# Kernel optimization log

Measured on AMD Instinct MI355X. Metric: run time of the kernel, lower is better.

## Reference

```python
import jax, jax.numpy as jnp
import numpy as np

OUT = (7, 7, 7)      # output_size (D_out, H_out, W_out)
SCALE = 1.0          # spatial_scale


def setup_inputs() -> dict:
    key = jax.random.key(0)
    k1, k2 = jax.random.split(key)
    B, C, D, H, W = 2, 256, 64, 64, 64
    N = 512
    features = jax.random.normal(k1, (B, C, D, H, W), dtype=jnp.float32)
    p = jax.random.uniform(k2, (B, N, 6), dtype=jnp.float32) * 63.0
    lo = jnp.minimum(p[..., :3], p[..., 3:])
    hi = jnp.maximum(p[..., :3], p[..., 3:])
    proposals = jnp.concatenate([lo, hi], axis=-1)  # (B, N, 6) valid boxes
    return {"features": features, "proposals": proposals}


def _trilinear(vol, gz, gy, gx):
    # vol: (C, D, H, W); gz/gy/gx: (Do, Ho, Wo) voxel-space coords.
    # grid_sample(mode='bilinear', padding_mode='zeros', align_corners=True)
    C, D, H, W = vol.shape
    z0f, y0f, x0f = jnp.floor(gz), jnp.floor(gy), jnp.floor(gx)
    wz, wy, wx = gz - z0f, gy - y0f, gx - x0f
    z0, y0, x0 = z0f.astype(jnp.int32), y0f.astype(jnp.int32), x0f.astype(jnp.int32)

    def gather(zi, yi, xi):
        valid = (zi >= 0) & (zi < D) & (yi >= 0) & (yi < H) & (xi >= 0) & (xi < W)
        v = vol[:, jnp.clip(zi, 0, D - 1), jnp.clip(yi, 0, H - 1), jnp.clip(xi, 0, W - 1)]
        return v * valid.astype(vol.dtype)[None]  # (C, Do, Ho, Wo)

    out = jnp.zeros((C,) + gz.shape, dtype=vol.dtype)
    for dz in (0, 1):
        for dy in (0, 1):
            for dx in (0, 1):
                w = ((wz if dz else 1.0 - wz)
                     * (wy if dy else 1.0 - wy)
                     * (wx if dx else 1.0 - wx))
                out = out + gather(z0 + dz, y0 + dy, x0 + dx) * w[None]
    return out


def reference(features, proposals):
    # features: (B, C, D, H, W); proposals: (B, N, 6) [x1,y1,z1,x2,y2,z2]
    B, C, D, H, W = features.shape
    Do, Ho, Wo = OUT

    def one_roi(vol, prop):
        p = prop * SCALE
        x1, y1, z1, x2, y2, z2 = p[0], p[1], p[2], p[3], p[4], p[5]
        zc = jnp.linspace(z1, z2, Do)
        yc = jnp.linspace(y1, y2, Ho)
        xc = jnp.linspace(x1, x2, Wo)
        gz, gy, gx = jnp.meshgrid(zc, yc, xc, indexing='ij')  # (Do,Ho,Wo)
        return _trilinear(vol, gz, gy, gx)  # (C, Do, Ho, Wo)

    per_batch = jax.vmap(lambda vol, props: jax.vmap(lambda p: one_roi(vol, p))(props))
    out = per_batch(features, proposals)  # (B, N, C, Do, Ho, Wo)
    return out.reshape(B * proposals.shape[1], C, Do, Ho, Wo)
```

## Files before the change

kernel.cpp:

```cpp
#include <hip/hip_runtime.h>
#include <hip/hip_fp16.h>


#define B_      2
#define C_      256
#define N_      512
#define NENT    (N_ * 7)
#define SP      66
#define THREADS 512
#define GROUPS  10
#define REC_F_BASE 128
#define WS_NEEDED ((size_t)REC_F_BASE * 4 + (size_t)B_ * NENT * 8 * 4)

typedef _Float16 h2v __attribute__((ext_vector_type(2)));

__device__ __forceinline__ float gcoord(float lo, float hi, int i) {
    return lo + (hi - lo) * (1.0f / 6.0f) * (float)i;
}

__device__ __forceinline__ uint32_t pkrtz(float a, float b) {
    auto h = __builtin_amdgcn_cvt_pkrtz(a, b);
    return __builtin_bit_cast(uint32_t, h);
}

__device__ __forceinline__ float xlerp(uint32_t pkv, uint32_t pkw) {
#if __has_builtin(__builtin_amdgcn_fdot2)
    return __builtin_amdgcn_fdot2(__builtin_bit_cast(h2v, pkv),
                                  __builtin_bit_cast(h2v, pkw), 0.0f, false);
#else
    h2v v = __builtin_bit_cast(h2v, pkv);
    h2v w = __builtin_bit_cast(h2v, pkw);
    return (float)v[0] * (float)w[0] + (float)v[1] * (float)w[1];
#endif
}

__global__ __launch_bounds__(256) void bucket_kernel(
    const float* __restrict__ props, int* __restrict__ wsi, float* __restrict__ wsf)
{
    int b = blockIdx.x;
    __shared__ int counts[63];
    __shared__ int starts[64];
    __shared__ int cursors[63];
    int tid = threadIdx.x;
    if (tid < 63) counts[tid] = 0;
    __syncthreads();
    for (int e = tid; e < NENT; e += 256) {
        int n = e / 7, iz = e - n * 7;
        const float* pr = props + (size_t)(b * N_ + n) * 6;
        float gz = gcoord(pr[2], pr[5], iz);
        int z0 = min(max((int)gz, 0), 62);
        atomicAdd(&counts[z0], 1);
    }
    __syncthreads();
    if (tid == 0) {
        int s = 0;
        for (int k = 0; k < 63; ++k) { starts[k] = s; s += counts[k]; }
        starts[63] = s;
    }
    __syncthreads();
    if (tid < 63) cursors[tid] = starts[tid];
    __syncthreads();
    for (int e = tid; e < NENT; e += 256) {
        int n = e / 7, iz = e - n * 7;
        const float* pr = props + (size_t)(b * N_ + n) * 6;
        float x1p = pr[0], y1p = pr[1], z1p = pr[2];
        float x2p = pr[3], y2p = pr[4], z2p = pr[5];
        float gz = gcoord(z1p, z2p, iz);
        int z0 = min(max((int)gz, 0), 62);
        float wz = gz - (float)z0;
        int pos = atomicAdd(&cursors[z0], 1);
        int off = (b * N_ + n) * (C_ * 343) + iz * 49;
        float* r = wsf + REC_F_BASE + (size_t)(b * NENT + pos) * 8;
        r[0] = x1p; r[1] = (x2p - x1p) * (1.0f / 6.0f);
        r[2] = y1p; r[3] = (y2p - y1p) * (1.0f / 6.0f);
        r[4] = wz;  r[5] = __int_as_float(off);
        r[6] = 0.0f; r[7] = 0.0f;
    }
    if (tid < 64) wsi[b * 64 + tid] = starts[tid];
}

__global__ __launch_bounds__(THREADS, 8) void roialign3d_small_kernel(
    const float* __restrict__ feat,
    const int* __restrict__ wsi,
    const float* __restrict__ wsf,
    float* __restrict__ out)
{
    __shared__ __align__(16) uint2 pk2[64 * SP];

    int bid = blockIdx.x;
    int s   = bid & 511;
    int z0  = bid >> 9;
    int b   = s >> 8;
    int c   = s & 255;
    int tid = threadIdx.x;

    int base = wsi[b * 64 + z0];
    int end  = wsi[b * 64 + z0 + 1];
    if (base == end) return;

    const float* vol = feat + ((size_t)s << 18) + ((size_t)z0 << 12);

    int y  = tid >> 3;
    int x8 = (tid & 7) << 3;
    const float* src = vol + y * 64 + x8;
    float4 p0a = *(const float4*)(src);
    float4 p0b = *(const float4*)(src + 4);
    float4 p1a = *(const float4*)(src + 4096);
    float4 p1b = *(const float4*)(src + 4100);

    int g = tid / 49;
    int p = tid - g * 49;
    int iy = p / 7;
    float fx = (float)(p - iy * 7);
    float fy = (float)iy;
    const float4* recs = (const float4*)(wsf + REC_F_BASE);
    const int rbase = b * NENT;
    int myEnd = (g < GROUPS) ? end : base;
    int e = base + g;
    float4 rA, rB, rAn, rBn;
    if (e < myEnd) {
        rA = recs[(size_t)(rbase + e) * 2];
        rB = recs[(size_t)(rbase + e) * 2 + 1];
        if (e + GROUPS < myEnd) {
            rAn = recs[(size_t)(rbase + e + GROUPS) * 2];
            rBn = recs[(size_t)(rbase + e + GROUPS) * 2 + 1];
        }
    }

    {
        float n0 = __shfl_down(p0a.x, 1);
        float n1 = __shfl_down(p1a.x, 1);
        uint4* d = (uint4*)&pk2[y * SP + x8];
        uint4 w0, w1, w2, w3;
        w0.x = pkrtz(p0a.x, p0a.y); w0.y = pkrtz(p1a.x, p1a.y);
        w0.z = pkrtz(p0a.y, p0a.z); w0.w = pkrtz(p1a.y, p1a.z);
        w1.x = pkrtz(p0a.z, p0a.w); w1.y = pkrtz(p1a.z, p1a.w);
        w1.z = pkrtz(p0a.w, p0b.x); w1.w = pkrtz(p1a.w, p1b.x);
        w2.x = pkrtz(p0b.x, p0b.y); w2.y = pkrtz(p1b.x, p1b.y);
        w2.z = pkrtz(p0b.y, p0b.z); w2.w = pkrtz(p1b.y, p1b.z);
        w3.x = pkrtz(p0b.z, p0b.w); w3.y = pkrtz(p1b.z, p1b.w);
        w3.z = pkrtz(p0b.w, n0);    w3.w = pkrtz(p1b.w, n1);
        d[0] = w0; d[1] = w1; d[2] = w2; d[3] = w3;
    }
    __syncthreads();

    float* outc = out + (size_t)c * 343;
    while (e < myEnd) {
        float gx = fmaf(rA.y, fx, rA.x);
        float gy = fmaf(rA.w, fy, rA.z);
        int x0 = (int)gx, y0 = (int)gy;
        float wx = __builtin_amdgcn_fractf(gx);
        float wy = __builtin_amdgcn_fractf(gy);
        uint32_t pw = pkrtz(1.0f - wx, wx);
        float wz = rB.x;
        int offc = __float_as_int(rB.y);
        int sl = y0 * SP + x0;
        uint2 q0 = pk2[sl];
        uint2 q1 = pk2[sl + SP];

        float4 tA = rAn, tB = rBn;
        int e2 = e + 2 * GROUPS;
        if (e2 < myEnd) {
            rAn = recs[(size_t)(rbase + e2) * 2];
            rBn = recs[(size_t)(rbase + e2) * 2 + 1];
        }

        float c00 = xlerp(q0.x, pw);
        float c10 = xlerp(q0.y, pw);
        float c01 = xlerp(q1.x, pw);
        float c11 = xlerp(q1.y, pw);
        float d0 = fmaf(c01 - c00, wy, c00);
        float d1 = fmaf(c11 - c10, wy, c10);
        outc[offc + p] = fmaf(d1 - d0, wz, d0);

        e += GROUPS; rA = tA; rB = tB;
    }
}

__global__ __launch_bounds__(128) void roialign3d_fallback(
    const float* __restrict__ feat, const float* __restrict__ props,
    float* __restrict__ out)
{
    int bid = blockIdx.x;
    int xcd = bid & 7;
    int j   = bid >> 3;
    int s   = xcd + ((j >> 9) << 3);
    int n   = j & 511;
    int b   = s >> 8;
    int c   = s & 255;
    const float* prop = props + ((size_t)(b * N_ + n)) * 6;
    float x1p = prop[0], y1p = prop[1], z1p = prop[2];
    float x2p = prop[3], y2p = prop[4], z2p = prop[5];
    float sx = (x2p - x1p) * (1.0f / 6.0f);
    float sy = (y2p - y1p) * (1.0f / 6.0f);
    float sz = (z2p - z1p) * (1.0f / 6.0f);
    const float* vol = feat + (size_t)s * (64 * 64 * 64);
    float* o = out + ((size_t)(b * N_ + n) * C_ + c) * 343;
    for (int p = threadIdx.x; p < 343; p += 128) {
        int iz = p / 49, r = p - iz * 49, iy = r / 7, ix = r - iy * 7;
        float gx = x1p + sx * ix, gy = y1p + sy * iy, gz = z1p + sz * iz;
        int x0 = (int)gx, y0 = (int)gy, z0 = (int)gz;
        float wx = gx - x0, wy = gy - y0, wz = gz - z0;
        int x1 = min(x0 + 1, 63), y1 = min(y0 + 1, 63), z1 = min(z0 + 1, 63);
        const float* p00 = vol + ((z0 * 64 + y0) << 6);
        const float* p01 = vol + ((z0 * 64 + y1) << 6);
        const float* p10 = vol + ((z1 * 64 + y0) << 6);
        const float* p11 = vol + ((z1 * 64 + y1) << 6);
        float c00 = p00[x0] + (p00[x1] - p00[x0]) * wx;
        float c01 = p01[x0] + (p01[x1] - p01[x0]) * wx;
        float c10 = p10[x0] + (p10[x1] - p10[x0]) * wx;
        float c11 = p11[x0] + (p11[x1] - p11[x0]) * wx;
        float d0 = c00 + (c01 - c00) * wy;
        float d1 = c10 + (c11 - c10) * wy;
        o[p] = d0 + (d1 - d0) * wz;
    }
}

extern "C" void kernel_launch(void* const* d_in, const int* in_sizes, int n_in,
                              void* d_out, int out_size, void* d_ws, size_t ws_size,
                              hipStream_t stream) {
    const float* feat  = (const float*)d_in[0];
    const float* props = (const float*)d_in[1];
    float* out = (float*)d_out;

    if (ws_size < WS_NEEDED) {
        roialign3d_fallback<<<B_ * C_ * N_, 128, 0, stream>>>(feat, props, out);
        return;
    }
    int*   wsi = (int*)d_ws;
    float* wsf = (float*)d_ws;
    bucket_kernel<<<B_, 256, 0, stream>>>(props, wsi, wsf);
    roialign3d_small_kernel<<<63 * 512, THREADS, 0, stream>>>(feat, wsi, wsf, out);
}
```

Measured before the change: 301.4 us.

## Map each thread to a full output row of seven x-samples per entry

The sampling kernel now gives each thread a whole 7-wide x-row of one (roi, z-slice) entry, instead of a single output voxel per thread with 10 groups of 49. Each wave covers 9 entries × 7 rows, so a 512-thread block handles 72 entries per iteration rather than 10. Since buckets average roughly 57 entries, most blocks should finish in one pass, with fewer record loads and less loop overhead, and the unrolled 7-point loop adds more independent work per thread. In exchange, each store instruction within a wave now writes addresses strided by 7 floats instead of contiguous ones, and register pressure rises.

```diff
diff --git a/kernel.cpp b/kernel.cpp
--- a/kernel.cpp
+++ b/kernel.cpp
@@ -8,7 +8,7 @@
 #define NENT    (N_ * 7)
 #define SP      66
 #define THREADS 512
-#define GROUPS  10
+#define EPP     72
 #define REC_F_BASE 128
 #define WS_NEEDED ((size_t)REC_F_BASE * 4 + (size_t)B_ * NENT * 8 * 4)
 
@@ -79,7 +79,7 @@
     if (tid < 64) wsi[b * 64 + tid] = starts[tid];
 }
 
-__global__ __launch_bounds__(THREADS, 8) void roialign3d_small_kernel(
+__global__ __launch_bounds__(THREADS, 8) void roialign3d_row_kernel(
     const float* __restrict__ feat,
     const int* __restrict__ wsi,
     const float* __restrict__ wsf,
@@ -108,22 +108,22 @@
     float4 p1a = *(const float4*)(src + 4096);
     float4 p1b = *(const float4*)(src + 4100);
 
-    int g = tid / 49;
-    int p = tid - g * 49;
-    int iy = p / 7;
-    float fx = (float)(p - iy * 7);
+    int wid  = tid >> 6;
+    int lane = tid & 63;
+    int g    = lane / 7;
+    int iy   = lane - g * 7;
     float fy = (float)iy;
     const float4* recs = (const float4*)(wsf + REC_F_BASE);
     const int rbase = b * NENT;
-    int myEnd = (g < GROUPS) ? end : base;
-    int e = base + g;
+    int myEnd = (lane < 63) ? end : base;
+    int e = base + wid * 9 + g;
     float4 rA, rB, rAn, rBn;
     if (e < myEnd) {
         rA = recs[(size_t)(rbase + e) * 2];
         rB = recs[(size_t)(rbase + e) * 2 + 1];
-        if (e + GROUPS < myEnd) {
-            rAn = recs[(size_t)(rbase + e + GROUPS) * 2];
-            rBn = recs[(size_t)(rbase + e + GROUPS) * 2 + 1];
+        if (e + EPP < myEnd) {
+            rAn = recs[(size_t)(rbase + e + EPP) * 2];
+            rBn = recs[(size_t)(rbase + e + EPP) * 2 + 1];
         }
     }
 
@@ -146,34 +146,41 @@
 
     float* outc = out + (size_t)c * 343;
     while (e < myEnd) {
-        float gx = fmaf(rA.y, fx, rA.x);
-        float gy = fmaf(rA.w, fy, rA.z);
-        int x0 = (int)gx, y0 = (int)gy;
-        float wx = __builtin_amdgcn_fractf(gx);
-        float wy = __builtin_amdgcn_fractf(gy);
-        uint32_t pw = pkrtz(1.0f - wx, wx);
-        float wz = rB.x;
-        int offc = __float_as_int(rB.y);
-        int sl = y0 * SP + x0;
-        uint2 q0 = pk2[sl];
-        uint2 q1 = pk2[sl + SP];
+        float gx0 = rA.x, sx = rA.y;
+        float gy  = fmaf(rA.w, fy, rA.z);
+        int   y0  = (int)gy;
+        float wy  = __builtin_amdgcn_fractf(gy);
+        float wz  = rB.x;
+        int  offc = __float_as_int(rB.y);
+        int slrow = y0 * SP;
+        float* od = outc + offc + iy * 7;
 
         float4 tA = rAn, tB = rBn;
-        int e2 = e + 2 * GROUPS;
+        int e2 = e + 2 * EPP;
         if (e2 < myEnd) {
             rAn = recs[(size_t)(rbase + e2) * 2];
             rBn = recs[(size_t)(rbase + e2) * 2 + 1];
         }
 
-        float c00 = xlerp(q0.x, pw);
-        float c10 = xlerp(q0.y, pw);
-        float c01 = xlerp(q1.x, pw);
-        float c11 = xlerp(q1.y, pw);
-        float d0 = fmaf(c01 - c00, wy, c00);
-        float d1 = fmaf(c11 - c10, wy, c10);
-        outc[offc + p] = fmaf(d1 - d0, wz, d0);
-
-        e += GROUPS; rA = tA; rB = tB;
+        #pragma unroll
+        for (int ix = 0; ix < 7; ++ix) {
+            float gx = fmaf(sx, (float)ix, gx0);
+            int   x0 = (int)gx;
+            float wx = __builtin_amdgcn_fractf(gx);
+            uint32_t pw = pkrtz(1.0f - wx, wx);
+            int sl = slrow + x0;
+            uint2 q0 = pk2[sl];
+            uint2 q1 = pk2[sl + SP];
+            float c00 = xlerp(q0.x, pw);
+            float c10 = xlerp(q0.y, pw);
+            float c01 = xlerp(q1.x, pw);
+            float c11 = xlerp(q1.y, pw);
+            float d0 = fmaf(c01 - c00, wy, c00);
+            float d1 = fmaf(c11 - c10, wy, c10);
+            od[ix] = fmaf(d1 - d0, wz, d0);
+        }
+
+        e += EPP; rA = tA; rB = tB;
     }
 }
 
@@ -230,5 +237,5 @@
     int*   wsi = (int*)d_ws;
     float* wsf = (float*)d_ws;
     bucket_kernel<<<B_, 256, 0, stream>>>(props, wsi, wsf);
-    roialign3d_small_kernel<<<63 * 512, THREADS, 0, stream>>>(feat, wsi, wsf, out);
-}
+    roialign3d_row_kernel<<<63 * 512, THREADS, 0, stream>>>(feat, wsi, wsf, out);
+}
```

Result: faster. 293.3 us (-2.7%).

## Stream z-planes through double-buffered LDS ring in one block per channel

Applied to the files above, without the earlier changes.

Replaces the grid of 63×512 blocks, one per (z-slab, channel), with one 1024-thread block per (batch, channel). Each block walks all 63 z-slabs, prefetching upcoming planes into registers and converting the next slab pair into a double-buffered LDS ring while the current slab's samples are computed. This loads each plane once instead of twice and removes per-block launch and setup overhead. The cost is far fewer blocks (512), so occupancy is low, and a barrier sits between every pair of slabs, which serialises work within each block.

```diff
diff --git a/kernel.cpp b/kernel.cpp
--- a/kernel.cpp
+++ b/kernel.cpp
@@ -7,8 +7,9 @@
 #define N_      512
 #define NENT    (N_ * 7)
 #define SP      66
-#define THREADS 512
-#define GROUPS  10
+#define PLANE_P (64 * SP)
+#define THREADS 1024
+#define GROUPS  20
 #define REC_F_BASE 128
 #define WS_NEEDED ((size_t)REC_F_BASE * 4 + (size_t)B_ * NENT * 8 * 4)
 
@@ -17,12 +18,10 @@
 __device__ __forceinline__ float gcoord(float lo, float hi, int i) {
     return lo + (hi - lo) * (1.0f / 6.0f) * (float)i;
 }
-
 __device__ __forceinline__ uint32_t pkrtz(float a, float b) {
     auto h = __builtin_amdgcn_cvt_pkrtz(a, b);
     return __builtin_bit_cast(uint32_t, h);
 }
-
 __device__ __forceinline__ float xlerp(uint32_t pkv, uint32_t pkw) {
 #if __has_builtin(__builtin_amdgcn_fdot2)
     return __builtin_amdgcn_fdot2(__builtin_bit_cast(h2v, pkv),
@@ -79,101 +78,116 @@
     if (tid < 64) wsi[b * 64 + tid] = starts[tid];
 }
 
-__global__ __launch_bounds__(THREADS, 8) void roialign3d_small_kernel(
+#define CONVERT(dstbase, A, Bv) do {                                        \
+        float n0_ = __shfl_down((A).x, 1);                                  \
+        float n1_ = __shfl_down((Bv).x, 1);                                 \
+        uint4 w0_, w1_;                                                     \
+        w0_.x = pkrtz((A).x, (A).y);  w0_.y = pkrtz((Bv).x, (Bv).y);        \
+        w0_.z = pkrtz((A).y, (A).z);  w0_.w = pkrtz((Bv).y, (Bv).z);        \
+        w1_.x = pkrtz((A).z, (A).w);  w1_.y = pkrtz((Bv).z, (Bv).w);        \
+        w1_.z = pkrtz((A).w, n0_);    w1_.w = pkrtz((Bv).w, n1_);           \
+        uint4* d_ = (uint4*)&(dstbase)[cy * SP + cx4];                      \
+        d_[0] = w0_; d_[1] = w1_;                                           \
+    } while (0)
+
+__global__ __launch_bounds__(THREADS, 8) void roialign3d_ring_kernel(
     const float* __restrict__ feat,
     const int* __restrict__ wsi,
     const float* __restrict__ wsf,
     float* __restrict__ out)
 {
-    __shared__ __align__(16) uint2 pk2[64 * SP];
-
-    int bid = blockIdx.x;
-    int s   = bid & 511;
-    int z0  = bid >> 9;
-    int b   = s >> 8;
-    int c   = s & 255;
+    __shared__ __align__(16) uint2 pk2[2 * PLANE_P];
+    __shared__ int starts[64];
+
+    int s = blockIdx.x;
+    int b = s >> 8;
+    int c = s & 255;
     int tid = threadIdx.x;
-
-    int base = wsi[b * 64 + z0];
-    int end  = wsi[b * 64 + z0 + 1];
-    if (base == end) return;
-
-    const float* vol = feat + ((size_t)s << 18) + ((size_t)z0 << 12);
-
-    int y  = tid >> 3;
-    int x8 = (tid & 7) << 3;
-    const float* src = vol + y * 64 + x8;
-    float4 p0a = *(const float4*)(src);
-    float4 p0b = *(const float4*)(src + 4);
-    float4 p1a = *(const float4*)(src + 4096);
-    float4 p1b = *(const float4*)(src + 4100);
+    const float4* pl = (const float4*)(feat + ((size_t)s << 18));
+
+    if (tid < 64) starts[tid] = wsi[b * 64 + tid];
+
+    float4 P0 = pl[tid];
+    float4 Pa = pl[1024 + tid];
+    float4 Pb = pl[2048 + tid];
+    float4 Pc = pl[3072 + tid];
+    float4 Pd;
+
+    int cy  = tid >> 4;
+    int cx4 = (tid & 15) << 2;
+    CONVERT(pk2, P0, Pa);
 
     int g = tid / 49;
     int p = tid - g * 49;
     int iy = p / 7;
     float fx = (float)(p - iy * 7);
     float fy = (float)iy;
-    const float4* recs = (const float4*)(wsf + REC_F_BASE);
-    const int rbase = b * NENT;
-    int myEnd = (g < GROUPS) ? end : base;
-    int e = base + g;
-    float4 rA, rB, rAn, rBn;
-    if (e < myEnd) {
-        rA = recs[(size_t)(rbase + e) * 2];
-        rB = recs[(size_t)(rbase + e) * 2 + 1];
-        if (e + GROUPS < myEnd) {
-            rAn = recs[(size_t)(rbase + e + GROUPS) * 2];
-            rBn = recs[(size_t)(rbase + e + GROUPS) * 2 + 1];
+    bool active = (g < GROUPS);
+    const float4* recs2 = (const float4*)(wsf + REC_F_BASE) + (size_t)(b * NENT) * 2;
+    float* outc = out + (size_t)c * 343;
+
+    asm volatile("s_waitcnt lgkmcnt(0)" ::: "memory");
+    __builtin_amdgcn_s_barrier();
+    asm volatile("" ::: "memory");
+
+    #pragma unroll 1
+    for (int z = 0; z < 63; ++z) {
+        if (z <= 59) Pd = pl[(size_t)(z + 4) * 1024 + tid];
+        __builtin_amdgcn_sched_barrier(0);
+
+        {
+            int base = starts[z];
+            int myEnd = active ? starts[z + 1] : base;
+            int e = base + g;
+            const uint2* slotz = pk2 + (z & 1) * PLANE_P;
+            float4 rA, rB, rAn, rBn;
+            if (e < myEnd) {
+                rA = recs2[(size_t)e * 2];
+                rB = recs2[(size_t)e * 2 + 1];
+                if (e + GROUPS < myEnd) {
+                    rAn = recs2[(size_t)(e + GROUPS) * 2];
+                    rBn = recs2[(size_t)(e + GROUPS) * 2 + 1];
+                }
+            }
+            while (e < myEnd) {
+                float gx = fmaf(rA.y, fx, rA.x);
+                float gy = fmaf(rA.w, fy, rA.z);
+                int x0 = (int)gx, y0 = (int)gy;
+                float wx = __builtin_amdgcn_fractf(gx);
+                float wy = __builtin_amdgcn_fractf(gy);
+                uint32_t pw = pkrtz(1.0f - wx, wx);
+                float wz = rB.x;
+                int offc = __float_as_int(rB.y);
+                int sl = y0 * SP + x0;
+                uint2 q0 = slotz[sl];
+                uint2 q1 = slotz[sl + SP];
+                float4 tA = rAn, tB = rBn;
+                int e2 = e + 2 * GROUPS;
+                if (e2 < myEnd) {
+                    rAn = recs2[(size_t)e2 * 2];
+                    rBn = recs2[(size_t)e2 * 2 + 1];
+                }
+                float c00 = xlerp(q0.x, pw);
+                float c10 = xlerp(q0.y, pw);
+                float c01 = xlerp(q1.x, pw);
+                float c11 = xlerp(q1.y, pw);
+                float d0 = fmaf(c01 - c00, wy, c00);
+                float d1 = fmaf(c11 - c10, wy, c10);
+                outc[offc + p] = fmaf(d1 - d0, wz, d0);
+                e += GROUPS; rA = tA; rB = tB;
+            }
         }
-    }
-
-    {
-        float n0 = __shfl_down(p0a.x, 1);
-        float n1 = __shfl_down(p1a.x, 1);
-        uint4* d = (uint4*)&pk2[y * SP + x8];
-        uint4 w0, w1, w2, w3;
-        w0.x = pkrtz(p0a.x, p0a.y); w0.y = pkrtz(p1a.x, p1a.y);
-        w0.z = pkrtz(p0a.y, p0a.z); w0.w = pkrtz(p1a.y, p1a.z);
-        w1.x = pkrtz(p0a.z, p0a.w); w1.y = pkrtz(p1a.z, p1a.w);
-        w1.z = pkrtz(p0a.w, p0b.x); w1.w = pkrtz(p1a.w, p1b.x);
-        w2.x = pkrtz(p0b.x, p0b.y); w2.y = pkrtz(p1b.x, p1b.y);
-        w2.z = pkrtz(p0b.y, p0b.z); w2.w = pkrtz(p1b.y, p1b.z);
-        w3.x = pkrtz(p0b.z, p0b.w); w3.y = pkrtz(p1b.z, p1b.w);
-        w3.z = pkrtz(p0b.w, n0);    w3.w = pkrtz(p1b.w, n1);
-        d[0] = w0; d[1] = w1; d[2] = w2; d[3] = w3;
-    }
-    __syncthreads();
-
-    float* outc = out + (size_t)c * 343;
-    while (e < myEnd) {
-        float gx = fmaf(rA.y, fx, rA.x);
-        float gy = fmaf(rA.w, fy, rA.z);
-        int x0 = (int)gx, y0 = (int)gy;
-        float wx = __builtin_amdgcn_fractf(gx);
-        float wy = __builtin_amdgcn_fractf(gy);
-        uint32_t pw = pkrtz(1.0f - wx, wx);
-        float wz = rB.x;
-        int offc = __float_as_int(rB.y);
-        int sl = y0 * SP + x0;
-        uint2 q0 = pk2[sl];
-        uint2 q1 = pk2[sl + SP];
-
-        float4 tA = rAn, tB = rBn;
-        int e2 = e + 2 * GROUPS;
-        if (e2 < myEnd) {
-            rAn = recs[(size_t)(rbase + e2) * 2];
-            rBn = recs[(size_t)(rbase + e2) * 2 + 1];
+
+        if (z <= 61)
+            CONVERT(pk2 + ((z + 1) & 1) * PLANE_P, Pa, Pb);
+
+        if (z < 62) {
+            asm volatile("s_waitcnt lgkmcnt(0)" ::: "memory");
+            __builtin_amdgcn_s_barrier();
+            asm volatile("" ::: "memory");
         }
 
-        float c00 = xlerp(q0.x, pw);
-        float c10 = xlerp(q0.y, pw);
-        float c01 = xlerp(q1.x, pw);
-        float c11 = xlerp(q1.y, pw);
-        float d0 = fmaf(c01 - c00, wy, c00);
-        float d1 = fmaf(c11 - c10, wy, c10);
-        outc[offc + p] = fmaf(d1 - d0, wz, d0);
-
-        e += GROUPS; rA = tA; rB = tB;
+        Pa = Pb; Pb = Pc; Pc = Pd;
     }
 }
 
@@ -230,5 +244,5 @@
     int*   wsi = (int*)d_ws;
     float* wsf = (float*)d_ws;
     bucket_kernel<<<B_, 256, 0, stream>>>(props, wsi, wsf);
-    roialign3d_small_kernel<<<63 * 512, THREADS, 0, stream>>>(feat, wsi, wsf, out);
-}
+    roialign3d_ring_kernel<<<B_ * C_, THREADS, 0, stream>>>(feat, wsi, wsf, out);
+}
```

Result: no change. 306.5 us (+1.7%).
